# Kernel tuning notes

Measured on AMD Instinct MI355X. Metric: run time of the kernel, lower is better.

The kernel has to match this reference:

```python
import jax, jax.numpy as jnp
import numpy as np

N_NODES = 50000
N_EDGES = 800000
IN_C = 128
OUT_C = 128
NEG_SLOPE = 0.2  # leaky_relu alpha


def setup_inputs() -> dict:
    key = jax.random.key(0)
    k1, k2, k3, k4 = jax.random.split(key, 4)
    h = jax.random.normal(k1, (N_NODES, IN_C), dtype=jnp.float32)
    edge_index = jax.random.randint(k2, (2, N_EDGES), 0, N_NODES, dtype=jnp.int64)
    # xavier_uniform with gain=1.414
    gW = 1.414 * np.sqrt(6.0 / (IN_C + OUT_C))
    W = jax.random.uniform(k3, (IN_C, OUT_C), dtype=jnp.float32, minval=-gW, maxval=gW)
    ga = 1.414 * np.sqrt(6.0 / (2 * OUT_C + 1))
    a = jax.random.uniform(k4, (2 * OUT_C, 1), dtype=jnp.float32, minval=-ga, maxval=ga)
    return {"h": h, "edge_index": edge_index, "W": W, "a": a}


def reference(h, edge_index, W, a):
    # eval mode (no dropout), concat=True -> ELU output
    Wh = h @ W                                  # [N, F]
    row, col = edge_index[0], edge_index[1]     # source, target
    F_out = W.shape[1]
    # cat([Wh_i, Wh_j]) @ a  ==  (Wh @ a_src)[row] + (Wh @ a_dst)[col]
    alpha_src = Wh @ a[:F_out, 0]               # [N]
    alpha_dst = Wh @ a[F_out:, 0]               # [N]
    edge_e = jax.nn.leaky_relu(alpha_src[row] + alpha_dst[col], negative_slope=NEG_SLOPE)  # [E]
    n = Wh.shape[0]
    # segment softmax over incoming edges of each target node
    m = jax.ops.segment_max(edge_e, col, num_segments=n)       # [N] (-inf for empty, never indexed)
    exp_e = jnp.exp(edge_e - m[col])                            # [E]
    s = jax.ops.segment_sum(exp_e, col, num_segments=n)         # [N]
    attn = exp_e / (s[col] + 1e-16)                              # [E]
    # scatter-add aggregation of attended source features
    h_prime = jax.ops.segment_sum(Wh[row] * attn[:, None], col, num_segments=n)  # [N, F]
    return jax.nn.elu(h_prime)
```

## Files before the change

### kernel.cpp

```cpp
#include <hip/hip_runtime.h>
#include <math.h>

#define NEG_BIG -1.0e30f
#define BSHIFT 8
#define MAXB 256

typedef __attribute__((ext_vector_type(8))) short short8v;
typedef __attribute__((ext_vector_type(4))) float f32x4;

__device__ __forceinline__ ushort f2bf(float f) {
  unsigned u = __float_as_uint(f);
  unsigned r = (u + 0x7fffu + ((u >> 16) & 1u)) >> 16;
  return (ushort)r;
}
__device__ __forceinline__ float bf_lo(unsigned u) { return __uint_as_float(u << 16); }
__device__ __forceinline__ float bf_hi(unsigned u) { return __uint_as_float(u & 0xffff0000u); }

__global__ void wprep_k(const float* __restrict__ W, ushort* __restrict__ Wbf,
                        int* __restrict__ bucket_count, int* __restrict__ done) {
  int j = blockIdx.x * blockDim.x + threadIdx.x;
  if (j < MAXB) bucket_count[j] = 0;
  if (j == 0) *done = 0;
  if (j >= 128 * 128) return;
  int i = j & 7;
  int l = (j >> 3) & 63;
  int n0 = (j >> 9) & 7;
  int kk = j >> 12;
  int k = kk * 32 + ((l >> 4) & 3) * 8 + i;
  int n = n0 * 16 + (l & 15);
  Wbf[j] = f2bf(W[k * 128 + n]);
}

__global__ __launch_bounds__(256) void histB_k(const void* __restrict__ ei, int E,
                                               unsigned* __restrict__ packed,
                                               int* __restrict__ bucket_count,
                                               int* __restrict__ done,
                                               int* __restrict__ bcur,
                                               int* __restrict__ bucket_base, int nblocks) {
  __shared__ int lh[MAXB];
  __shared__ int wsum[4];
  __shared__ int last;
  int tid = (int)threadIdx.x;
  lh[tid] = 0;
  __syncthreads();

  const int* p32 = (const int*)ei;
  bool is64 = true;
#pragma unroll
  for (int i = 0; i < 32; ++i) is64 = is64 && (p32[2 * i + 1] == 0);
  const long long* p64 = (const long long*)ei;
  int stride = gridDim.x * 256;
  for (int e = blockIdx.x * 256 + tid; e < E; e += stride) {
    int r, c;
    if (is64) { r = (int)p64[e]; c = (int)p64[E + e]; }
    else      { r = p32[e];      c = p32[E + e]; }
    packed[e] = ((unsigned)c << 16) | (unsigned)r;
    atomicAdd(&lh[c >> BSHIFT], 1);
  }
  __syncthreads();
  if (lh[tid]) atomicAdd(&bucket_count[tid], lh[tid]);
  __syncthreads();
  if (tid == 0) {
    __threadfence();
    int old = atomicAdd(done, 1);
    last = (old == nblocks - 1);
  }
  __syncthreads();
  if (!last) return;
  __threadfence();

  int lane = tid & 63, wid = tid >> 6;
  int v = atomicAdd(&bucket_count[tid], 0);
  int x = v;
#pragma unroll
  for (int off = 1; off < 64; off <<= 1) {
    int t = __shfl_up(x, off);
    if (lane >= off) x += t;
  }
  if (lane == 63) wsum[wid] = x;
  __syncthreads();
  int woff = 0;
  for (int w = 0; w < wid; ++w) woff += wsum[w];
  int excl = woff + x - v;
  bcur[tid] = excl;
  bucket_base[tid] = excl;
  if (tid == 255) bucket_base[256] = excl + v;
}

__global__ __launch_bounds__(256) void gemm_wh(const float* __restrict__ h,
                                               const ushort* __restrict__ Wbf,
                                               const float* __restrict__ a,
                                               ushort* __restrict__ Whb,
                                               float* __restrict__ asrc,
                                               float* __restrict__ adst, int N) {
  int tid = (int)threadIdx.x;
  int w = tid >> 6;
  int l = tid & 63;
  int lg = l >> 4;
  int lm = l & 15;
  int r0 = blockIdx.x * 64 + 16 * w;
  const short8v* Wb8 = (const short8v*)Wbf;

  float as_v[8], ad_v[8];
#pragma unroll
  for (int n0 = 0; n0 < 8; ++n0) {
    as_v[n0] = a[n0 * 16 + lm];
    ad_v[n0] = a[128 + n0 * 16 + lm];
  }

  f32x4 acc[8];
#pragma unroll
  for (int n0 = 0; n0 < 8; ++n0) acc[n0] = (f32x4){0.f, 0.f, 0.f, 0.f};

  int arow = r0 + lm;
  const float* hrow = h + (size_t)arow * 128;
  bool rok = (arow < N);

#pragma unroll
  for (int kk = 0; kk < 4; ++kk) {
    short8v av;
    if (rok) {
      const float4* hp = (const float4*)(hrow + kk * 32 + lg * 8);
      float4 x0 = hp[0], x1 = hp[1];
      av[0] = (short)f2bf(x0.x); av[1] = (short)f2bf(x0.y);
      av[2] = (short)f2bf(x0.z); av[3] = (short)f2bf(x0.w);
      av[4] = (short)f2bf(x1.x); av[5] = (short)f2bf(x1.y);
      av[6] = (short)f2bf(x1.z); av[7] = (short)f2bf(x1.w);
    } else {
      av = (short8v){0, 0, 0, 0, 0, 0, 0, 0};
    }
#pragma unroll
    for (int n0 = 0; n0 < 8; ++n0) {
      short8v bv = Wb8[(kk * 8 + n0) * 64 + l];
      acc[n0] = __builtin_amdgcn_mfma_f32_16x16x32_bf16(av, bv, acc[n0], 0, 0, 0);
    }
  }

#pragma unroll
  for (int reg = 0; reg < 4; ++reg) {
    int r = r0 + lg * 4 + reg;
    if (r < N) {
      short8v pk;
#pragma unroll
      for (int n0 = 0; n0 < 8; ++n0) pk[n0] = (short)f2bf(acc[n0][reg]);
      *(short8v*)(Whb + (size_t)r * 128 + lm * 8) = pk;
    }
  }

#pragma unroll
  for (int reg = 0; reg < 4; ++reg) {
    float ps = 0.f, pd = 0.f;
#pragma unroll
    for (int n0 = 0; n0 < 8; ++n0) {
      ps += acc[n0][reg] * as_v[n0];
      pd += acc[n0][reg] * ad_v[n0];
    }
#pragma unroll
    for (int off = 1; off < 16; off <<= 1) {
      ps += __shfl_xor(ps, off);
      pd += __shfl_xor(pd, off);
    }
    int r = r0 + lg * 4 + reg;
    if (lm == 0 && r < N) { asrc[r] = ps; adst[r] = pd; }
  }
}

#define TILE 8192
__global__ __launch_bounds__(1024) void bin_k(const unsigned* __restrict__ packed,
                                              int* __restrict__ bcur,
                                              unsigned* __restrict__ bin_buf, int E) {
  __shared__ int lhist[MAXB];
  __shared__ int lbase[MAXB];
  int tid = (int)threadIdx.x;
  int t0 = blockIdx.x * TILE;

  if (tid < MAXB) lhist[tid] = 0;
  __syncthreads();

  unsigned rec[8];
  int rb[8], rr[8];
#pragma unroll
  for (int k = 0; k < 8; ++k) {
    int i = t0 + tid + k * 1024;
    rb[k] = -1;
    if (i < E) {
      rec[k] = packed[i];
      rb[k] = (int)(rec[k] >> (16 + BSHIFT));
      rr[k] = atomicAdd(&lhist[rb[k]], 1);
    }
  }
  __syncthreads();
  if (tid < MAXB) lbase[tid] = lhist[tid] ? atomicAdd(&bcur[tid], lhist[tid]) : 0;
  __syncthreads();
#pragma unroll
  for (int k = 0; k < 8; ++k) {
    if (rb[k] >= 0) bin_buf[lbase[rb[k]] + rr[k]] = rec[k];
  }
}

__global__ __launch_bounds__(1024) void perm3_k(const unsigned* __restrict__ bin_buf,
                                                const int* __restrict__ bucket_base,
                                                int* __restrict__ rowptr,
                                                ushort* __restrict__ row_sorted,
                                                int N, int nbuckets) {
  __shared__ int hist[MAXB];
  __shared__ int cur[MAXB];
  __shared__ int wsum[16];
  int b = blockIdx.x;
  int tid = (int)threadIdx.x;
  int c0 = b << BSHIFT;
  int ncol = min(MAXB, N - c0);
  int e0 = bucket_base[b], e1 = bucket_base[b + 1];

  if (tid < MAXB) hist[tid] = 0;
  __syncthreads();
  for (int i = e0 + tid; i < e1; i += 1024) {
    int cl = (int)(bin_buf[i] >> 16) - c0;
    if ((unsigned)cl < (unsigned)MAXB) atomicAdd(&hist[cl], 1);
  }
  __syncthreads();

  int lane = tid & 63, wid = tid >> 6;
  int v = (tid < MAXB) ? hist[tid] : 0;
  int x = v;
#pragma unroll
  for (int off = 1; off < 64; off <<= 1) {
    int t = __shfl_up(x, off);
    if (lane >= off) x += t;
  }
  if (lane == 63) wsum[wid] = x;
  __syncthreads();
  if (tid < MAXB) {
    int woff = 0;
    for (int w = 0; w < wid; ++w) woff += wsum[w];
    int excl = woff + x - v;
    cur[tid] = e0 + excl;
    if (tid < ncol) rowptr[c0 + tid] = e0 + excl;
  }
  if (b == nbuckets - 1 && tid == 0) rowptr[N] = e1;
  __syncthreads();

  for (int i = e0 + tid; i < e1; i += 1024) {
    unsigned rec = bin_buf[i];
    int cl = (int)(rec >> 16) - c0;
    if ((unsigned)cl < (unsigned)MAXB) {
      int p = atomicAdd(&cur[cl], 1);
      row_sorted[p] = (ushort)(rec & 0xffffu);
    }
  }
}

__global__ __launch_bounds__(256) void softagg_k(const int* __restrict__ rowptr,
                                                 const ushort* __restrict__ row_sorted,
                                                 const float* __restrict__ asrc,
                                                 const float* __restrict__ adst,
                                                 const ushort* __restrict__ Whb,
                                                 float* __restrict__ out, int N) {
  int node = blockIdx.x * 4 + ((int)threadIdx.x >> 6);
  if (node >= N) return;
  int lane = (int)threadIdx.x & 63;
  int beg = rowptr[node], end = rowptr[node + 1];
  int deg = end - beg;
  float adc = adst[node];
  float ax = 0.f, ay = 0.f;

  if (deg <= 64) {
    int r = 0;
    float v = NEG_BIG;
    if (lane < deg) {
      r = row_sorted[beg + lane];
      v = asrc[r] + adc;
      v = (v >= 0.f) ? v : 0.2f * v;
    }
    float m = v;
#pragma unroll
    for (int off = 32; off > 0; off >>= 1) m = fmaxf(m, __shfl_xor(m, off));
    float e = (lane < deg) ? expf(v - m) : 0.f;
    float s = e;
#pragma unroll
    for (int off = 32; off > 0; off >>= 1) s += __shfl_xor(s, off);
    float w = e / (s + 1e-16f);

    int j = 0;
    for (; j + 7 < deg; j += 8) {
      float wv[8];
      int rv[8];
#pragma unroll
      for (int q = 0; q < 8; ++q) { wv[q] = __shfl(w, j + q); rv[q] = __shfl(r, j + q); }
      unsigned u[8];
#pragma unroll
      for (int q = 0; q < 8; ++q) u[q] = ((const unsigned*)(Whb + (size_t)rv[q] * 128))[lane];
#pragma unroll
      for (int q = 0; q < 8; ++q) { ax += wv[q] * bf_lo(u[q]); ay += wv[q] * bf_hi(u[q]); }
    }
    for (; j < deg; ++j) {
      float wj = __shfl(w, j);
      int rj = __shfl(r, j);
      unsigned u = ((const unsigned*)(Whb + (size_t)rj * 128))[lane];
      ax += wj * bf_lo(u); ay += wj * bf_hi(u);
    }
  } else {
    float m = NEG_BIG, s = 0.f;
    for (int i = beg + lane; i < end; i += 64) {
      float v = asrc[row_sorted[i]] + adc;
      v = (v >= 0.f) ? v : 0.2f * v;
      if (v > m) { s = s * expf(m - v) + 1.f; m = v; }
      else       { s += expf(v - m); }
    }
#pragma unroll
    for (int off = 32; off > 0; off >>= 1) {
      float mo = __shfl_xor(m, off);
      float so = __shfl_xor(s, off);
      float M = fmaxf(m, mo);
      s = s * expf(m - M) + so * expf(mo - M);
      m = M;
    }
    float inv = 1.f / (s + 1e-16f);
    for (int i = beg; i < end; ++i) {
      int rj = row_sorted[i];
      float v = asrc[rj] + adc;
      v = (v >= 0.f) ? v : 0.2f * v;
      float wj = expf(v - m) * inv;
      unsigned u = ((const unsigned*)(Whb + (size_t)rj * 128))[lane];
      ax += wj * bf_lo(u); ay += wj * bf_hi(u);
    }
  }

  ax = ax > 0.f ? ax : expm1f(ax);
  ay = ay > 0.f ? ay : expm1f(ay);
  int c0 = ((lane & 3) << 5) + (lane >> 2);
  float* orow = out + (size_t)node * 128;
  orow[c0] = ax;
  orow[c0 + 16] = ay;
}

extern "C" void kernel_launch(void* const* d_in, const int* in_sizes, int n_in,
                              void* d_out, int out_size, void* d_ws, size_t ws_size,
                              hipStream_t stream) {
  const float* h = (const float*)d_in[0];
  const void* ei = d_in[1];
  const float* W = (const float*)d_in[2];
  const float* a = (const float*)d_in[3];
  int N = in_sizes[0] / 128;
  int E = in_sizes[1] / 2;
  float* out = (float*)d_out;

  ushort* Whb = (ushort*)d_ws;
  float* asrc = (float*)(Whb + (size_t)N * 128);
  float* adst = asrc + N;
  int* bucket_count = (int*)(adst + N);
  int* done = bucket_count + MAXB;
  int* bcur = done + 4;
  int* bucket_base = bcur + MAXB;
  int* rowptr = bucket_base + MAXB + 4;
  unsigned* bin_buf = (unsigned*)(rowptr + N + 1);
  unsigned* packed = bin_buf + E;
  ushort* row_sorted = (ushort*)(packed + E);
  ushort* Wbf = row_sorted + E;

  int nbuckets = (N + MAXB - 1) >> BSHIFT;
  const int HBLOCKS = 256;

  wprep_k<<<64, 256, 0, stream>>>(W, Wbf, bucket_count, done);
  histB_k<<<HBLOCKS, 256, 0, stream>>>(ei, E, packed, bucket_count, done, bcur, bucket_base, HBLOCKS);
  gemm_wh<<<(N + 63) / 64, 256, 0, stream>>>(h, Wbf, a, Whb, asrc, adst, N);
  bin_k<<<(E + TILE - 1) / TILE, 1024, 0, stream>>>(packed, bcur, bin_buf, E);
  perm3_k<<<nbuckets, 1024, 0, stream>>>(bin_buf, bucket_base, rowptr, row_sorted, N, nbuckets);
  softagg_k<<<(N + 3) / 4, 256, 0, stream>>>(rowptr, row_sorted, asrc, adst, Whb, out, N);
}
```

Before: 93.49 us.

## Merge histogram and GEMM into one launch; use fast exp in softmax

The edge histogram/packing kernel and the Wh GEMM kernel are merged into a single launch, with block index deciding which role a block plays. The two independent stages can then run concurrently across CUs, and one launch boundary is removed. Separately, expf is replaced by __expf in the segment-softmax aggregation, trading accuracy for cheaper transcendental evaluation. The merged kernel may raise register pressure for the histogram blocks, since it now shares a binary with the GEMM path.

```diff
diff --git a/kernel.cpp b/kernel.cpp
--- a/kernel.cpp
+++ b/kernel.cpp
@@ -31,74 +31,73 @@
   Wbf[j] = f2bf(W[k * 128 + n]);
 }
 
-__global__ __launch_bounds__(256) void histB_k(const void* __restrict__ ei, int E,
-                                               unsigned* __restrict__ packed,
-                                               int* __restrict__ bucket_count,
-                                               int* __restrict__ done,
-                                               int* __restrict__ bcur,
-                                               int* __restrict__ bucket_base, int nblocks) {
+__global__ __launch_bounds__(256) void hist_gemm_k(
+    const void* __restrict__ ei, int E,
+    unsigned* __restrict__ packed, int* __restrict__ bucket_count,
+    int* __restrict__ done, int* __restrict__ bcur, int* __restrict__ bucket_base,
+    int hblocks,
+    const float* __restrict__ h, const ushort* __restrict__ Wbf,
+    const float* __restrict__ a, ushort* __restrict__ Whb,
+    float* __restrict__ asrc, float* __restrict__ adst, int N) {
   __shared__ int lh[MAXB];
   __shared__ int wsum[4];
   __shared__ int last;
   int tid = (int)threadIdx.x;
-  lh[tid] = 0;
-  __syncthreads();
-
-  const int* p32 = (const int*)ei;
-  bool is64 = true;
-#pragma unroll
-  for (int i = 0; i < 32; ++i) is64 = is64 && (p32[2 * i + 1] == 0);
-  const long long* p64 = (const long long*)ei;
-  int stride = gridDim.x * 256;
-  for (int e = blockIdx.x * 256 + tid; e < E; e += stride) {
-    int r, c;
-    if (is64) { r = (int)p64[e]; c = (int)p64[E + e]; }
-    else      { r = p32[e];      c = p32[E + e]; }
-    packed[e] = ((unsigned)c << 16) | (unsigned)r;
-    atomicAdd(&lh[c >> BSHIFT], 1);
-  }
-  __syncthreads();
-  if (lh[tid]) atomicAdd(&bucket_count[tid], lh[tid]);
-  __syncthreads();
-  if (tid == 0) {
+
+  if ((int)blockIdx.x < hblocks) {
+    lh[tid] = 0;
+    __syncthreads();
+
+    const int* p32 = (const int*)ei;
+    bool is64 = true;
+#pragma unroll
+    for (int i = 0; i < 32; ++i) is64 = is64 && (p32[2 * i + 1] == 0);
+    const long long* p64 = (const long long*)ei;
+    int stride = hblocks * 256;
+    for (int e = blockIdx.x * 256 + tid; e < E; e += stride) {
+      int r, c;
+      if (is64) { r = (int)p64[e]; c = (int)p64[E + e]; }
+      else      { r = p32[e];      c = p32[E + e]; }
+      packed[e] = ((unsigned)c << 16) | (unsigned)r;
+      atomicAdd(&lh[c >> BSHIFT], 1);
+    }
+    __syncthreads();
+    if (lh[tid]) atomicAdd(&bucket_count[tid], lh[tid]);
+    __syncthreads();
+    if (tid == 0) {
+      __threadfence();
+      int old = atomicAdd(done, 1);
+      last = (old == hblocks - 1);
+    }
+    __syncthreads();
+    if (!last) return;
     __threadfence();
-    int old = atomicAdd(done, 1);
-    last = (old == nblocks - 1);
-  }
-  __syncthreads();
-  if (!last) return;
-  __threadfence();
-
-  int lane = tid & 63, wid = tid >> 6;
-  int v = atomicAdd(&bucket_count[tid], 0);
-  int x = v;
-#pragma unroll
-  for (int off = 1; off < 64; off <<= 1) {
-    int t = __shfl_up(x, off);
-    if (lane >= off) x += t;
-  }
-  if (lane == 63) wsum[wid] = x;
-  __syncthreads();
-  int woff = 0;
-  for (int w = 0; w < wid; ++w) woff += wsum[w];
-  int excl = woff + x - v;
-  bcur[tid] = excl;
-  bucket_base[tid] = excl;
-  if (tid == 255) bucket_base[256] = excl + v;
-}
-
-__global__ __launch_bounds__(256) void gemm_wh(const float* __restrict__ h,
-                                               const ushort* __restrict__ Wbf,
-                                               const float* __restrict__ a,
-                                               ushort* __restrict__ Whb,
-                                               float* __restrict__ asrc,
-                                               float* __restrict__ adst, int N) {
-  int tid = (int)threadIdx.x;
+
+    int lane = tid & 63, wid = tid >> 6;
+    int v = atomicAdd(&bucket_count[tid], 0);
+    int x = v;
+#pragma unroll
+    for (int off = 1; off < 64; off <<= 1) {
+      int t = __shfl_up(x, off);
+      if (lane >= off) x += t;
+    }
+    if (lane == 63) wsum[wid] = x;
+    __syncthreads();
+    int woff = 0;
+    for (int w = 0; w < wid; ++w) woff += wsum[w];
+    int excl = woff + x - v;
+    bcur[tid] = excl;
+    bucket_base[tid] = excl;
+    if (tid == 255) bucket_base[256] = excl + v;
+    return;
+  }
+
+  int gb = (int)blockIdx.x - hblocks;
   int w = tid >> 6;
   int l = tid & 63;
   int lg = l >> 4;
   int lm = l & 15;
-  int r0 = blockIdx.x * 64 + 16 * w;
+  int r0 = gb * 64 + 16 * w;
   const short8v* Wb8 = (const short8v*)Wbf;
 
   float as_v[8], ad_v[8];
@@ -275,7 +274,7 @@
     float m = v;
 #pragma unroll
     for (int off = 32; off > 0; off >>= 1) m = fmaxf(m, __shfl_xor(m, off));
-    float e = (lane < deg) ? expf(v - m) : 0.f;
+    float e = (lane < deg) ? __expf(v - m) : 0.f;
     float s = e;
 #pragma unroll
     for (int off = 32; off > 0; off >>= 1) s += __shfl_xor(s, off);
@@ -304,15 +303,15 @@
     for (int i = beg + lane; i < end; i += 64) {
       float v = asrc[row_sorted[i]] + adc;
       v = (v >= 0.f) ? v : 0.2f * v;
-      if (v > m) { s = s * expf(m - v) + 1.f; m = v; }
-      else       { s += expf(v - m); }
+      if (v > m) { s = s * __expf(m - v) + 1.f; m = v; }
+      else       { s += __expf(v - m); }
     }
 #pragma unroll
     for (int off = 32; off > 0; off >>= 1) {
       float mo = __shfl_xor(m, off);
       float so = __shfl_xor(s, off);
       float M = fmaxf(m, mo);
-      s = s * expf(m - M) + so * expf(mo - M);
+      s = s * __expf(m - M) + so * __expf(mo - M);
       m = M;
     }
     float inv = 1.f / (s + 1e-16f);
@@ -320,7 +319,7 @@
       int rj = row_sorted[i];
       float v = asrc[rj] + adc;
       v = (v >= 0.f) ? v : 0.2f * v;
-      float wj = expf(v - m) * inv;
+      float wj = __expf(v - m) * inv;
       unsigned u = ((const unsigned*)(Whb + (size_t)rj * 128))[lane];
       ax += wj * bf_lo(u); ay += wj * bf_hi(u);
     }
@@ -360,10 +359,12 @@
 
   int nbuckets = (N + MAXB - 1) >> BSHIFT;
   const int HBLOCKS = 256;
+  int gblocks = (N + 63) / 64;
 
   wprep_k<<<64, 256, 0, stream>>>(W, Wbf, bucket_count, done);
-  histB_k<<<HBLOCKS, 256, 0, stream>>>(ei, E, packed, bucket_count, done, bcur, bucket_base, HBLOCKS);
-  gemm_wh<<<(N + 63) / 64, 256, 0, stream>>>(h, Wbf, a, Whb, asrc, adst, N);
+  hist_gemm_k<<<HBLOCKS + gblocks, 256, 0, stream>>>(
+      ei, E, packed, bucket_count, done, bcur, bucket_base, HBLOCKS,
+      h, Wbf, a, Whb, asrc, adst, N);
   bin_k<<<(E + TILE - 1) / TILE, 1024, 0, stream>>>(packed, bcur, bin_buf, E);
   perm3_k<<<nbuckets, 1024, 0, stream>>>(bin_buf, bucket_base, rowptr, row_sorted, N, nbuckets);
   softagg_k<<<(N + 3) / 4, 256, 0, stream>>>(rowptr, row_sorted, asrc, adst, Whb, out, N);
```

After: 90.29 us. -3.4%, faster.
